# Kernel tuning notes

Measured on AMD Instinct MI355X. Metric: run time of the kernel, lower is better.

## Reference

```python
import jax, jax.numpy as jnp
import numpy as np

B, L, H, HEADS = 4, 256, 256, 4
D = H // HEADS
NEG = jnp.float32(-2.0**32 + 1)


def setup_inputs() -> dict:
    key = jax.random.key(0)
    ks = jax.random.split(key, 16)
    inp = {
        "queries": jax.random.normal(ks[0], (B, L, H), jnp.float32),
        "keys": jax.random.normal(ks[1], (B, L, H), jnp.float32),
        "values": jax.random.normal(ks[2], (B, L, H), jnp.float32),
        "time_matrix_K": jax.random.normal(ks[3], (B, L, L, H), jnp.float32),
        "time_matrix_V": jax.random.normal(ks[4], (B, L, L, H), jnp.float32),
        "abs_pos_K": jax.random.normal(ks[5], (B, L, H), jnp.float32),
        "abs_pos_V": jax.random.normal(ks[6], (B, L, H), jnp.float32),
        "time_mask": jax.random.randint(ks[7], (B, L), 0, 2) == 1,
        "future_time_mask": jnp.triu(jnp.ones((L, L), bool), k=1),
        # linear layer params (torch Linear: y = x @ W.T + b)
        "Wq": jax.random.normal(ks[8], (H, H), jnp.float32) / np.sqrt(H),
        "bq": jax.random.normal(ks[9], (H,), jnp.float32) * 0.01,
        "Wk": jax.random.normal(ks[10], (H, H), jnp.float32) / np.sqrt(H),
        "bk": jax.random.normal(ks[11], (H,), jnp.float32) * 0.01,
        "Wv": jax.random.normal(ks[12], (H, H), jnp.float32) / np.sqrt(H),
        "bv": jax.random.normal(ks[13], (H,), jnp.float32) * 0.01,
    }
    return inp


def _split_heads(x):  # [B,L,H] -> [h,B,L,d]
    b, l, _ = x.shape
    return x.reshape(b, l, HEADS, D).transpose(2, 0, 1, 3)


def _split_heads_rel(t):  # [B,L,L,H] -> [h,B,L,L,d]
    b, l, _, _ = t.shape
    return t.reshape(b, l, l, HEADS, D).transpose(3, 0, 1, 2, 4)


def reference(queries, keys, values, time_matrix_K, time_matrix_V,
              abs_pos_K, abs_pos_V, time_mask, future_time_mask,
              Wq, bq, Wk, bk, Wv, bv):
    Q = _split_heads(queries @ Wq.T + bq)   # [h,B,L,d]
    K = _split_heads(keys @ Wk.T + bk)
    V = _split_heads(values @ Wv.T + bv)
    tK = _split_heads_rel(time_matrix_K)    # [h,B,L,L,d]
    tV = _split_heads_rel(time_matrix_V)
    pK = _split_heads(abs_pos_K)            # [h,B,L,d]
    pV = _split_heads(abs_pos_V)

    scores = jnp.einsum("hbqd,hbkd->hbqk", Q, K)
    scores += jnp.einsum("hbqd,hbkd->hbqk", Q, pK)
    scores += jnp.einsum("hbqkd,hbqd->hbqk", tK, Q)
    scores = scores / jnp.sqrt(jnp.float32(D))

    mask = time_mask[None, :, :, None] | future_time_mask[None, None, :, :]
    scores = jnp.where(mask, NEG, scores)
    attn = jax.nn.softmax(scores, axis=-1)  # [h,B,L,L]  (dropout: eval mode)

    out = jnp.einsum("hbqk,hbkd->hbqd", attn, V)
    out += jnp.einsum("hbqk,hbkd->hbqd", attn, pV)
    out += jnp.einsum("hbqk,hbqkd->hbqd", attn, tV)
    # merge heads: [h,B,L,d] -> [B,L,H]
    return out.transpose(1, 2, 0, 3).reshape(B, L, H)
```

## Files before the change

### kernel.cpp

```cpp
#include <hip/hip_runtime.h>
#include <math.h>
#include <stdint.h>

#define LSEQ 256
#define HD 256

typedef float floatx4 __attribute__((ext_vector_type(4)));

__device__ __forceinline__ float dot4(float4 a, float4 b) {
    return a.x * b.x + a.y * b.y + a.z * b.z + a.w * b.w;
}
__device__ __forceinline__ float4 ldnt4(const float* p) {
    floatx4 r = __builtin_nontemporal_load((const floatx4*)p);
    return make_float4(r.x, r.y, r.z, r.w);
}

#define LOAD8NT(R, base, kk) do { _Pragma("unroll") \
    for (int j = 0; j < 8; ++j) R[j] = ldnt4((base) + (size_t)((kk) + j) * HD + le4); } while (0)
#define LOAD8P(R, base, kk) do { _Pragma("unroll") \
    for (int j = 0; j < 8; ++j) R[j] = *(const float4*)((base) + (size_t)((kk) + j) * HD + le4); } while (0)

#define CONS8_K1(R, kk) do { _Pragma("unroll") \
    for (int j = 0; j < 8; ++j) { \
        float s = dot4(q4, R[j]); \
        s += __shfl_xor(s, 1); s += __shfl_xor(s, 2); \
        s += __shfl_xor(s, 4); s += __shfl_xor(s, 8); \
        if ((lane & 15) == 0) scK[head][(kk) + j] = s; } } while (0)
#define CONS8_K2(R, kk) do { _Pragma("unroll") \
    for (int j = 0; j < 8; ++j) { \
        float s = dot4(q4, R[j]); \
        s += __shfl_xor(s, 1); s += __shfl_xor(s, 2); \
        s += __shfl_xor(s, 4); s += __shfl_xor(s, 8); \
        if ((lane & 15) == 0) sc[head][(kk) + j] = (s + scK[head][(kk) + j]) * 0.125f; } } while (0)
#define CONS8_V(R, kk) do { _Pragma("unroll") \
    for (int j = 0; j < 8; ++j) { \
        float a = sc[head][(kk) + j]; \
        acc.x += a * R[j].x; acc.y += a * R[j].y; \
        acc.z += a * R[j].z; acc.w += a * R[j].w; } } while (0)
#define CONS8_S(R, kk) do { _Pragma("unroll") \
    for (int j = 0; j < 8; ++j) { \
        acc.x += R[j].x; acc.y += R[j].y; acc.z += R[j].z; acc.w += R[j].w; } } while (0)

#define PIPE(LOADM, CONSM, CONS1, base, r0v, rendv) do { \
    int n_ = (rendv) > (r0v) ? (rendv) - (r0v) : 0; \
    int k_ = (r0v); \
    float4 A_[8], B_[8]; \
    if (n_ >= 8) { \
        LOADM(A_, base, k_); \
        if (n_ >= 16) { \
            LOADM(B_, base, k_ + 8); CONSM(A_, k_); \
            if (n_ >= 24) { \
                LOADM(A_, base, k_ + 16); CONSM(B_, k_ + 8); \
                if (n_ >= 32) { \
                    LOADM(B_, base, k_ + 24); CONSM(A_, k_ + 16); CONSM(B_, k_ + 24); \
                } else { CONSM(A_, k_ + 16); } \
            } else { CONSM(B_, k_ + 8); } \
        } else { CONSM(A_, k_); } \
        k_ += (n_ & ~7); \
    } \
    for (int jj = 0; jj < (n_ & 7); ++jj, ++k_) { \
        float4 T_ = *(const float4*)((base) + (size_t)k_ * HD + le4); \
        CONS1(T_, k_); \
    } } while (0)

#define CONS1_K1(T, kk) do { \
    float s = dot4(q4, T); \
    s += __shfl_xor(s, 1); s += __shfl_xor(s, 2); \
    s += __shfl_xor(s, 4); s += __shfl_xor(s, 8); \
    if ((lane & 15) == 0) scK[head][kk] = s; } while (0)
#define CONS1_K2(T, kk) do { \
    float s = dot4(q4, T); \
    s += __shfl_xor(s, 1); s += __shfl_xor(s, 2); \
    s += __shfl_xor(s, 4); s += __shfl_xor(s, 8); \
    if ((lane & 15) == 0) sc[head][kk] = (s + scK[head][kk]) * 0.125f; } while (0)
#define CONS1_V(T, kk) do { \
    float a = sc[head][kk]; \
    acc.x += a * T.x; acc.y += a * T.y; acc.z += a * T.z; acc.w += a * T.w; } while (0)
#define CONS1_S(T, kk) do { \
    acc.x += T.x; acc.y += T.y; acc.z += T.z; acc.w += T.w; } while (0)

__global__ __launch_bounds__(256) void proj_kernel(
    const float* __restrict__ queries, const float* __restrict__ keys,
    const float* __restrict__ values,
    const float* __restrict__ apK, const float* __restrict__ apV,
    const float* __restrict__ Wq, const float* __restrict__ bq,
    const float* __restrict__ Wk, const float* __restrict__ bk,
    const float* __restrict__ Wv, const float* __restrict__ bv,
    float* __restrict__ Qo, float* __restrict__ Ko, float* __restrict__ Vo)
{
    const int R = 4;
    int tid = threadIdx.x;
    int row0 = blockIdx.x * R;

    float aq[R] = {0.f, 0.f, 0.f, 0.f};
    float ak[R] = {0.f, 0.f, 0.f, 0.f};
    float av[R] = {0.f, 0.f, 0.f, 0.f};

    const float* wq = Wq + tid * HD;
    const float* wk = Wk + tid * HD;
    const float* wv = Wv + tid * HD;

    #pragma unroll 2
    for (int i = 0; i < HD; i += 4) {
        float4 wq4 = *(const float4*)(wq + i);
        float4 wk4 = *(const float4*)(wk + i);
        float4 wv4 = *(const float4*)(wv + i);
        #pragma unroll
        for (int r = 0; r < R; ++r) {
            float4 xq = *(const float4*)(queries + (row0 + r) * HD + i);
            float4 xk = *(const float4*)(keys    + (row0 + r) * HD + i);
            float4 xv = *(const float4*)(values  + (row0 + r) * HD + i);
            aq[r] += dot4(xq, wq4);
            ak[r] += dot4(xk, wk4);
            av[r] += dot4(xv, wv4);
        }
    }
    #pragma unroll
    for (int r = 0; r < R; ++r) {
        int idx = (row0 + r) * HD + tid;
        Qo[idx] = aq[r] + bq[tid];
        Ko[idx] = ak[r] + bk[tid] + apK[idx];
        Vo[idx] = av[r] + bv[tid] + apV[idx];
    }
}

__global__ __launch_bounds__(256) void vmean_kernel(
    const float* __restrict__ Veff, float* __restrict__ Vm)
{
    int b = blockIdx.x;
    int t = threadIdx.x;
    const float* Vb = Veff + b * (LSEQ * HD);
    float s = 0.f;
    #pragma unroll 4
    for (int k = 0; k < LSEQ; ++k)
        s += Vb[k * HD + t];
    Vm[b * HD + t] = s * (1.0f / 256.0f);
}

__global__ __launch_bounds__(512, 2) void attn_kernel(
    const float* __restrict__ Q, const float* __restrict__ Keff,
    const float* __restrict__ Veff, const float* __restrict__ tK,
    const float* __restrict__ tV, const float* __restrict__ Vm,
    const int* __restrict__ tmask, float* __restrict__ out)
{
    __shared__ float scK[4][260];
    __shared__ float sc[4][260];
    __shared__ float outp[8][256];

    int bid = blockIdx.x;
    int q = 255 - (bid >> 2);
    int b = bid & 3;
    int bq = (b << 8) | q;

    int tid = threadIdx.x;
    int w = tid >> 6;
    int lane = tid & 63;
    int head = lane >> 4;
    int le4 = lane * 4;

    bool masked = tmask[bq] != 0;

    const float* tVr = tV + (size_t)bq * (LSEQ * HD);
    float4 acc = make_float4(0.f, 0.f, 0.f, 0.f);

    if (masked) {
        int r0 = w * 32;
        PIPE(LOAD8NT, CONS8_S, CONS1_S, tVr, r0, r0 + 32);
    } else {
        const float* tKr = tK + (size_t)bq * (LSEQ * HD);
        const float* Kb  = Keff + b * (LSEQ * HD);
        const float* Vb  = Veff + b * (LSEQ * HD);
        float4 q4 = *(const float4*)(Q + bq * HD + le4);

        int nk = q + 1;
        int run = (nk + 7) >> 3;
        int r0 = w * run;
        int rend = min(r0 + run, nk);

        PIPE(LOAD8P, CONS8_K1, CONS1_K1, Kb, r0, rend);
        PIPE(LOAD8NT, CONS8_K2, CONS1_K2, tKr, r0, rend);
        __syncthreads();

        if (w < 4) {
            int k0 = lane * 4;
            float4 vv = *(const float4*)(&sc[w][k0]);
            float x0 = (k0 + 0 <= q) ? vv.x : -INFINITY;
            float x1 = (k0 + 1 <= q) ? vv.y : -INFINITY;
            float x2 = (k0 + 2 <= q) ? vv.z : -INFINITY;
            float x3 = (k0 + 3 <= q) ? vv.w : -INFINITY;
            float m = fmaxf(fmaxf(x0, x1), fmaxf(x2, x3));
            #pragma unroll
            for (int off = 32; off >= 1; off >>= 1)
                m = fmaxf(m, __shfl_xor(m, off));
            float e0 = __expf(x0 - m);
            float e1 = __expf(x1 - m);
            float e2 = __expf(x2 - m);
            float e3 = __expf(x3 - m);
            float ssum = e0 + e1 + e2 + e3;
            #pragma unroll
            for (int off = 32; off >= 1; off >>= 1)
                ssum += __shfl_xor(ssum, off);
            float inv = 1.0f / ssum;
            *(float4*)(&sc[w][k0]) = make_float4(e0 * inv, e1 * inv,
                                                 e2 * inv, e3 * inv);
        }
        __syncthreads();

        PIPE(LOAD8NT, CONS8_V, CONS1_V, tVr, r0, rend);
        PIPE(LOAD8P, CONS8_V, CONS1_V, Vb, r0, rend);
    }

    *(float4*)(&outp[w][le4]) = acc;
    __syncthreads();
    if (tid < 256) {
        float o = 0.f;
        #pragma unroll
        for (int p = 0; p < 8; ++p) o += outp[p][tid];
        if (masked) o = o * (1.0f / 256.0f) + Vm[b * HD + tid];
        out[(size_t)bq * HD + tid] = o;
    }
}

extern "C" void kernel_launch(void* const* d_in, const int* in_sizes, int n_in,
                              void* d_out, int out_size, void* d_ws, size_t ws_size,
                              hipStream_t stream) {
    const float* queries = (const float*)d_in[0];
    const float* keys    = (const float*)d_in[1];
    const float* values  = (const float*)d_in[2];
    const float* tK      = (const float*)d_in[3];
    const float* tV      = (const float*)d_in[4];
    const float* apK     = (const float*)d_in[5];
    const float* apV     = (const float*)d_in[6];
    const int*   tmask   = (const int*)d_in[7];
    const float* Wq = (const float*)d_in[9];
    const float* bq = (const float*)d_in[10];
    const float* Wk = (const float*)d_in[11];
    const float* bk = (const float*)d_in[12];
    const float* Wv = (const float*)d_in[13];
    const float* bv = (const float*)d_in[14];

    float* ws = (float*)d_ws;
    float* Qo = ws;
    float* Ko = ws + 262144;
    float* Vo = ws + 524288;
    float* Vm = ws + 786432;
    float* out = (float*)d_out;

    proj_kernel<<<256, 256, 0, stream>>>(queries, keys, values, apK, apV,
                                         Wq, bq, Wk, bk, Wv, bv, Qo, Ko, Vo);
    vmean_kernel<<<4, 256, 0, stream>>>(Vo, Vm);
    attn_kernel<<<1024, 512, 0, stream>>>(Qo, Ko, Vo, tK, tV, Vm, tmask, out);
}
```

Baseline: 102.8 us.

## Shrink attention blocks to four waves with looped double-buffered row pipeline

The attention kernel now runs 256 threads (4 waves) per query row instead of 512, so each wave streams a longer run of key rows. The fixed 8-row load batches become a looped 4+4 double-buffered pipeline that covers any run length. Nontemporal loads are replaced by plain loads, and the separate scK buffer is folded into sc. The aim is higher occupancy with fewer registers and less shared memory per block; in exchange each wave has a longer serial stream, and dropping nontemporal hints may add cache pollution.

```diff
diff --git a/kernel.cpp b/kernel.cpp
--- a/kernel.cpp
+++ b/kernel.cpp
@@ -5,74 +5,64 @@
 #define LSEQ 256
 #define HD 256
 
-typedef float floatx4 __attribute__((ext_vector_type(4)));
-
 __device__ __forceinline__ float dot4(float4 a, float4 b) {
     return a.x * b.x + a.y * b.y + a.z * b.z + a.w * b.w;
 }
-__device__ __forceinline__ float4 ldnt4(const float* p) {
-    floatx4 r = __builtin_nontemporal_load((const floatx4*)p);
-    return make_float4(r.x, r.y, r.z, r.w);
-}
-
-#define LOAD8NT(R, base, kk) do { _Pragma("unroll") \
-    for (int j = 0; j < 8; ++j) R[j] = ldnt4((base) + (size_t)((kk) + j) * HD + le4); } while (0)
-#define LOAD8P(R, base, kk) do { _Pragma("unroll") \
-    for (int j = 0; j < 8; ++j) R[j] = *(const float4*)((base) + (size_t)((kk) + j) * HD + le4); } while (0)
-
-#define CONS8_K1(R, kk) do { _Pragma("unroll") \
-    for (int j = 0; j < 8; ++j) { \
+
+#define LOAD4(R, base, kk) do { _Pragma("unroll") \
+    for (int j = 0; j < 4; ++j) R[j] = *(const float4*)((base) + (size_t)((kk) + j) * HD + le4); } while (0)
+
+#define CONS4_K1(R, kk) do { _Pragma("unroll") \
+    for (int j = 0; j < 4; ++j) { \
         float s = dot4(q4, R[j]); \
         s += __shfl_xor(s, 1); s += __shfl_xor(s, 2); \
         s += __shfl_xor(s, 4); s += __shfl_xor(s, 8); \
-        if ((lane & 15) == 0) scK[head][(kk) + j] = s; } } while (0)
-#define CONS8_K2(R, kk) do { _Pragma("unroll") \
-    for (int j = 0; j < 8; ++j) { \
+        if ((lane & 15) == 0) sc[head][(kk) + j] = s; } } while (0)
+#define CONS4_K2(R, kk) do { _Pragma("unroll") \
+    for (int j = 0; j < 4; ++j) { \
         float s = dot4(q4, R[j]); \
         s += __shfl_xor(s, 1); s += __shfl_xor(s, 2); \
         s += __shfl_xor(s, 4); s += __shfl_xor(s, 8); \
-        if ((lane & 15) == 0) sc[head][(kk) + j] = (s + scK[head][(kk) + j]) * 0.125f; } } while (0)
-#define CONS8_V(R, kk) do { _Pragma("unroll") \
-    for (int j = 0; j < 8; ++j) { \
+        if ((lane & 15) == 0) sc[head][(kk) + j] = (s + sc[head][(kk) + j]) * 0.125f; } } while (0)
+#define CONS4_V(R, kk) do { _Pragma("unroll") \
+    for (int j = 0; j < 4; ++j) { \
         float a = sc[head][(kk) + j]; \
         acc.x += a * R[j].x; acc.y += a * R[j].y; \
         acc.z += a * R[j].z; acc.w += a * R[j].w; } } while (0)
-#define CONS8_S(R, kk) do { _Pragma("unroll") \
-    for (int j = 0; j < 8; ++j) { \
+#define CONS4_S(R, kk) do { _Pragma("unroll") \
+    for (int j = 0; j < 4; ++j) { \
         acc.x += R[j].x; acc.y += R[j].y; acc.z += R[j].z; acc.w += R[j].w; } } while (0)
 
-#define PIPE(LOADM, CONSM, CONS1, base, r0v, rendv) do { \
-    int n_ = (rendv) > (r0v) ? (rendv) - (r0v) : 0; \
-    int k_ = (r0v); \
-    float4 A_[8], B_[8]; \
-    if (n_ >= 8) { \
-        LOADM(A_, base, k_); \
-        if (n_ >= 16) { \
-            LOADM(B_, base, k_ + 8); CONSM(A_, k_); \
-            if (n_ >= 24) { \
-                LOADM(A_, base, k_ + 16); CONSM(B_, k_ + 8); \
-                if (n_ >= 32) { \
-                    LOADM(B_, base, k_ + 24); CONSM(A_, k_ + 16); CONSM(B_, k_ + 24); \
-                } else { CONSM(A_, k_ + 16); } \
-            } else { CONSM(B_, k_ + 8); } \
-        } else { CONSM(A_, k_); } \
-        k_ += (n_ & ~7); \
-    } \
-    for (int jj = 0; jj < (n_ & 7); ++jj, ++k_) { \
-        float4 T_ = *(const float4*)((base) + (size_t)k_ * HD + le4); \
-        CONS1(T_, k_); \
+#define PIPE4(CONSM, CONS1, base, r0v, rendv) do { \
+    if ((rendv) > (r0v)) { \
+        int nfull_ = ((rendv) - (r0v)) & ~7; \
+        int kend8_ = (r0v) + nfull_; \
+        float4 A_[4], B_[4]; \
+        if (nfull_ >= 8) { \
+            LOAD4(A_, base, (r0v)); LOAD4(B_, base, (r0v) + 4); \
+            int k_ = (r0v); \
+            for (; k_ + 16 <= kend8_; k_ += 8) { \
+                CONSM(A_, k_);     LOAD4(A_, base, k_ + 8); \
+                CONSM(B_, k_ + 4); LOAD4(B_, base, k_ + 12); \
+            } \
+            CONSM(A_, k_); CONSM(B_, k_ + 4); \
+        } \
+        for (int k_ = kend8_; k_ < (rendv); ++k_) { \
+            float4 T_ = *(const float4*)((base) + (size_t)k_ * HD + le4); \
+            CONS1(T_, k_); \
+        } \
     } } while (0)
 
 #define CONS1_K1(T, kk) do { \
     float s = dot4(q4, T); \
     s += __shfl_xor(s, 1); s += __shfl_xor(s, 2); \
     s += __shfl_xor(s, 4); s += __shfl_xor(s, 8); \
-    if ((lane & 15) == 0) scK[head][kk] = s; } while (0)
+    if ((lane & 15) == 0) sc[head][kk] = s; } while (0)
 #define CONS1_K2(T, kk) do { \
     float s = dot4(q4, T); \
     s += __shfl_xor(s, 1); s += __shfl_xor(s, 2); \
     s += __shfl_xor(s, 4); s += __shfl_xor(s, 8); \
-    if ((lane & 15) == 0) sc[head][kk] = (s + scK[head][kk]) * 0.125f; } while (0)
+    if ((lane & 15) == 0) sc[head][kk] = (s + sc[head][kk]) * 0.125f; } while (0)
 #define CONS1_V(T, kk) do { \
     float a = sc[head][kk]; \
     acc.x += a * T.x; acc.y += a * T.y; acc.z += a * T.z; acc.w += a * T.w; } while (0)
@@ -137,15 +127,14 @@
     Vm[b * HD + t] = s * (1.0f / 256.0f);
 }
 
-__global__ __launch_bounds__(512, 2) void attn_kernel(
+__global__ __launch_bounds__(256, 8) void attn_kernel(
     const float* __restrict__ Q, const float* __restrict__ Keff,
     const float* __restrict__ Veff, const float* __restrict__ tK,
     const float* __restrict__ tV, const float* __restrict__ Vm,
     const int* __restrict__ tmask, float* __restrict__ out)
 {
-    __shared__ float scK[4][260];
     __shared__ float sc[4][260];
-    __shared__ float outp[8][256];
+    __shared__ float outp[4][256];
 
     int bid = blockIdx.x;
     int q = 255 - (bid >> 2);
@@ -164,8 +153,9 @@
     float4 acc = make_float4(0.f, 0.f, 0.f, 0.f);
 
     if (masked) {
-        int r0 = w * 32;
-        PIPE(LOAD8NT, CONS8_S, CONS1_S, tVr, r0, r0 + 32);
+        int r0 = w * 64;
+        int rend = r0 + 64;
+        PIPE4(CONS4_S, CONS1_S, tVr, r0, rend);
     } else {
         const float* tKr = tK + (size_t)bq * (LSEQ * HD);
         const float* Kb  = Keff + b * (LSEQ * HD);
@@ -173,15 +163,15 @@
         float4 q4 = *(const float4*)(Q + bq * HD + le4);
 
         int nk = q + 1;
-        int run = (nk + 7) >> 3;
-        int r0 = w * run;
+        int run = (nk + 3) >> 2;
+        int r0 = min(w * run, nk);
         int rend = min(r0 + run, nk);
 
-        PIPE(LOAD8P, CONS8_K1, CONS1_K1, Kb, r0, rend);
-        PIPE(LOAD8NT, CONS8_K2, CONS1_K2, tKr, r0, rend);
+        PIPE4(CONS4_K1, CONS1_K1, Kb, r0, rend);
+        PIPE4(CONS4_K2, CONS1_K2, tKr, r0, rend);
         __syncthreads();
 
-        if (w < 4) {
+        {
             int k0 = lane * 4;
             float4 vv = *(const float4*)(&sc[w][k0]);
             float x0 = (k0 + 0 <= q) ? vv.x : -INFINITY;
@@ -206,16 +196,14 @@
         }
         __syncthreads();
 
-        PIPE(LOAD8NT, CONS8_V, CONS1_V, tVr, r0, rend);
-        PIPE(LOAD8P, CONS8_V, CONS1_V, Vb, r0, rend);
+        PIPE4(CONS4_V, CONS1_V, tVr, r0, rend);
+        PIPE4(CONS4_V, CONS1_V, Vb, r0, rend);
     }
 
     *(float4*)(&outp[w][le4]) = acc;
     __syncthreads();
     if (tid < 256) {
-        float o = 0.f;
-        #pragma unroll
-        for (int p = 0; p < 8; ++p) o += outp[p][tid];
+        float o = outp[0][tid] + outp[1][tid] + outp[2][tid] + outp[3][tid];
         if (masked) o = o * (1.0f / 256.0f) + Vm[b * HD + tid];
         out[(size_t)bq * HD + tid] = o;
     }
@@ -249,5 +237,5 @@
     proj_kernel<<<256, 256, 0, stream>>>(queries, keys, values, apK, apV,
                                          Wq, bq, Wk, bk, Wv, bv, Qo, Ko, Vo);
     vmean_kernel<<<4, 256, 0, stream>>>(Vo, Vm);
-    attn_kernel<<<1024, 512, 0, stream>>>(Qo, Ko, Vo, tK, tV, Vm, tmask, out);
-}
+    attn_kernel<<<1024, 256, 0, stream>>>(Qo, Ko, Vo, tK, tV, Vm, tmask, out);
+}
```

Result: slower. 162.2 us (+57.8%).
